# Performance work log

Measured on AMD Instinct MI355X. Metric: run time of the kernel, lower is better.

Reference implementation:

```python
import jax, jax.numpy as jnp
import numpy as np

N_HEAD = 16

def setup_inputs() -> dict:
    key = jax.random.key(0)
    k0, k1, k2, k3, k4 = jax.random.split(key, 5)
    B, T, C = 4, 2048, 1024
    x = jax.random.normal(k0, (B, T, C), dtype=jnp.float32)
    # torch nn.Linear weights are (out_features, in_features); scale like kaiming-uniform-ish
    s = 1.0 / np.sqrt(C)
    Wk = jax.random.uniform(k1, (C, C), jnp.float32, -s, s)
    Wq = jax.random.uniform(k2, (C, C), jnp.float32, -s, s)
    Wv = jax.random.uniform(k3, (C, C), jnp.float32, -s, s)
    Wo = jax.random.uniform(k4, (C, C), jnp.float32, -s, s)
    return {"x": x, "Wk": Wk, "Wq": Wq, "Wv": Wv, "Wo": Wo}

def reference(x, Wk, Wq, Wv, Wo):
    B, T, C = x.shape
    hs = C // N_HEAD
    # projections (torch Linear: y = x @ W.T), split heads -> (B, nh, T, hs)
    def proj(W):
        return (x @ W.T).reshape(B, T, N_HEAD, hs).transpose(0, 2, 1, 3)
    k = proj(Wk)
    q = proj(Wq)
    v = proj(Wv)
    # dot attention: scale by sqrt(head_dim) (k.shape[2] after transpose in source)
    score = jnp.einsum('bhqd,bhkd->bhqk', q, k) / jnp.sqrt(jnp.asarray(hs, x.dtype))
    # NOTE: source calls score.masked_fill(mask, -inf) without assignment -> mask has no effect.
    e = jax.nn.softmax(score, axis=-1)
    o = jnp.einsum('bhqk,bhkd->bhqd', e, v)          # (B, nh, T, hs)
    o = o.transpose(0, 2, 1, 3).reshape(B, T, C)     # merge heads
    o = o @ Wo.T                                      # final projection
    # dropout is identity in eval mode
    return o
```

## Files before the change

kernel.cpp:

```cpp
#include <hip/hip_runtime.h>
#include <hip/hip_bf16.h>
#include <cstddef>
#include <cstdint>

#define B_DIM 4
#define T_DIM 2048
#define C_DIM 1024
#define NHEAD 16
#define HS    64
#define QKV_LD 3072

#define QSCALE 0.18033688011112042f

typedef __attribute__((ext_vector_type(8))) short short8;
typedef __attribute__((ext_vector_type(4))) short short4v;
typedef __attribute__((ext_vector_type(4))) float f32x4;

__device__ __forceinline__ short f2bf(float x) {
    __hip_bfloat16 b = __float2bfloat16(x);
    return *reinterpret_cast<short*>(&b);
}

__device__ __forceinline__ void load_lds16(const void* g, void* l) {
    __builtin_amdgcn_global_load_lds(
        (const __attribute__((address_space(1))) void*)(g),
        (__attribute__((address_space(3))) void*)(l),
        16, 0, 0);
}

#define XBLK 4096
#define WBLK 512

__global__ __launch_bounds__(256) void cast_all(
    const float* __restrict__ x,
    const float* __restrict__ wq, const float* __restrict__ wk,
    const float* __restrict__ wv, const float* __restrict__ wo,
    short* __restrict__ xb, short* __restrict__ wout)
{
    const int bid = blockIdx.x;
    const float* in;
    short* out;
    float scale;
    int i;
    if (bid < XBLK) {
        i = bid * 256 + threadIdx.x;
        in = x; out = xb; scale = 1.0f;
    } else {
        const int r = bid - XBLK;
        const int sel = r >> 9;
        i = (r & (WBLK - 1)) * 256 + threadIdx.x;
        in  = (sel == 0) ? wq : (sel == 1) ? wk : (sel == 2) ? wv : wo;
        out = wout + (size_t)sel * (WBLK * 256 * 8);
        scale = (sel == 0) ? QSCALE : 1.0f;
    }
    const float4* p = (const float4*)in + (size_t)i * 2;
    float4 a = p[0], b = p[1];
    short8 o;
    o[0]=f2bf(a.x*scale); o[1]=f2bf(a.y*scale); o[2]=f2bf(a.z*scale); o[3]=f2bf(a.w*scale);
    o[4]=f2bf(b.x*scale); o[5]=f2bf(b.y*scale); o[6]=f2bf(b.z*scale); o[7]=f2bf(b.w*scale);
    *((short8*)out + i) = o;
}

template<int OUT_MODE>
__global__ __launch_bounds__(512, 2) void gemm_bt_8ph(
    const short* __restrict__ A,
    const short* __restrict__ Bm,
    void* __restrict__ Cm,
    short* __restrict__ Vt,
    int M, int N, int K)
{
    __shared__ __align__(16) short lds[49152];

    const int nbx = N >> 8;
    int wg = blockIdx.x;
    const int cpx = gridDim.x >> 3;
    wg = (wg & 7) * cpx + (wg >> 3);
    const int bx = wg % nbx, by = wg / nbx;
    const int m0 = by << 7, n0 = bx << 8;

    const int t = threadIdx.x;
    const int w = t >> 6, lane = t & 63;
    const int l16 = lane & 15, quad = lane >> 4;
    const int wm = w >> 2, wn = w & 3;

    const int rcall  = t >> 3;
    const int schunk = (t & 7) ^ (rcall & 7);
    const int dstoff = w * 512;

    const short* Ag = A  + (size_t)(m0 + rcall) * K + schunk * 8;
    const short* Bg = Bm + (size_t)(n0 + rcall) * K + schunk * 8;

    short* const Ab0 = lds;
    short* const Ab1 = lds + 8192;
    short* const Bb0 = lds + 16384;
    short* const Bb1 = lds + 32768;

    int aoff[4][2], boff[4][2];
    #pragma unroll
    for (int mf = 0; mf < 4; ++mf) {
        const int ar = wm * 64 + mf * 16 + l16;
        #pragma unroll
        for (int ks = 0; ks < 2; ++ks)
            aoff[mf][ks] = ar * 64 + (((ks * 4 + quad) ^ (ar & 7)) * 8);
    }
    #pragma unroll
    for (int nf = 0; nf < 4; ++nf) {
        const int br = wn * 64 + nf * 16 + l16;
        #pragma unroll
        for (int ks = 0; ks < 2; ++ks)
            boff[nf][ks] = br * 64 + (((ks * 4 + quad) ^ (br & 7)) * 8);
    }

    f32x4 acc[4][4];
    const f32x4 zero4 = {0.f, 0.f, 0.f, 0.f};
    #pragma unroll
    for (int mf = 0; mf < 4; ++mf)
        #pragma unroll
        for (int nf = 0; nf < 4; ++nf) acc[mf][nf] = zero4;

    const int NT = K >> 6;

    #define ST64(gb, kt, ro, lb)                                               \
        load_lds16((gb) + (size_t)(ro) * K + (size_t)(kt) * 64,                \
                   (lb) + (ro) * 64 + dstoff)

    ST64(Ag, 0, 0, Ab0); ST64(Ag, 0, 64, Ab0);
    ST64(Bg, 0, 0, Bb0); ST64(Bg, 0, 64, Bb0);
    ST64(Bg, 0, 128, Bb0); ST64(Bg, 0, 192, Bb0);
    ST64(Ag, 1, 0, Ab1); ST64(Ag, 1, 64, Ab1);

    for (int kt = 0; kt < NT; ++kt) {
        short* Acur = (kt & 1) ? Ab1 : Ab0;
        short* Bcur = (kt & 1) ? Bb1 : Bb0;
        short* Bnx  = (kt & 1) ? Bb0 : Bb1;

        if (kt == NT - 1) asm volatile("s_waitcnt vmcnt(0)" ::: "memory");
        else              asm volatile("s_waitcnt vmcnt(2)" ::: "memory");
        __builtin_amdgcn_s_barrier();

        short8 bfr[4][2], af[2][2];
        #pragma unroll
        for (int nf = 0; nf < 4; ++nf)
            #pragma unroll
            for (int ks = 0; ks < 2; ++ks)
                bfr[nf][ks] = *(const short8*)(Bcur + boff[nf][ks]);
        #pragma unroll
        for (int mf = 0; mf < 2; ++mf)
            #pragma unroll
            for (int ks = 0; ks < 2; ++ks)
                af[mf][ks] = *(const short8*)(Acur + aoff[mf][ks]);

        if (kt + 1 < NT) { ST64(Bg, kt + 1, 0, Bnx); ST64(Bg, kt + 1, 64, Bnx); }

        __builtin_amdgcn_s_barrier();
        __builtin_amdgcn_s_setprio(1);
        #pragma unroll
        for (int mf = 0; mf < 2; ++mf)
            #pragma unroll
            for (int nf = 0; nf < 4; ++nf)
                #pragma unroll
                for (int ks = 0; ks < 2; ++ks)
                    acc[mf][nf] = __builtin_amdgcn_mfma_f32_16x16x32_bf16(
                        af[mf][ks], bfr[nf][ks], acc[mf][nf], 0, 0, 0);
        __builtin_amdgcn_s_setprio(0);
        __builtin_amdgcn_s_barrier();

        short8 af2[2][2];
        #pragma unroll
        for (int mf = 0; mf < 2; ++mf)
            #pragma unroll
            for (int ks = 0; ks < 2; ++ks)
                af2[mf][ks] = *(const short8*)(Acur + aoff[2 + mf][ks]);

        if (kt + 1 < NT) { ST64(Bg, kt + 1, 128, Bnx); ST64(Bg, kt + 1, 192, Bnx); }

        __builtin_amdgcn_s_barrier();
        __builtin_amdgcn_s_setprio(1);
        #pragma unroll
        for (int mf = 0; mf < 2; ++mf)
            #pragma unroll
            for (int nf = 0; nf < 4; ++nf)
                #pragma unroll
                for (int ks = 0; ks < 2; ++ks)
                    acc[2 + mf][nf] = __builtin_amdgcn_mfma_f32_16x16x32_bf16(
                        af2[mf][ks], bfr[nf][ks], acc[2 + mf][nf], 0, 0, 0);
        __builtin_amdgcn_s_setprio(0);
        __builtin_amdgcn_s_barrier();

        if (kt + 2 < NT) {
            short* Aw = (kt & 1) ? Ab1 : Ab0;
            ST64(Ag, kt + 2, 0, Aw); ST64(Ag, kt + 2, 64, Aw);
        }
    }
    #undef ST64

    if (OUT_MODE == 2 && n0 >= 2 * C_DIM) {
        const int b    = m0 >> 11;
        const int tt0  = (m0 & 2047) + wm * 64 + quad * 4;
        #pragma unroll
        for (int nf = 0; nf < 4; ++nf) {
            const int vcol = (n0 - 2 * C_DIM) + wn * 64 + nf * 16 + l16;
            const int h    = vcol >> 6;
            const int d    = vcol & 63;
            short* dcol = Vt + ((size_t)((b << 4) + h) * HS + d) * T_DIM;
            #pragma unroll
            for (int mf = 0; mf < 4; ++mf) {
                const int tt = tt0 + mf * 16;
                short4v o;
                o[0] = f2bf(acc[mf][nf][0]); o[1] = f2bf(acc[mf][nf][1]);
                o[2] = f2bf(acc[mf][nf][2]); o[3] = f2bf(acc[mf][nf][3]);
                *(short4v*)(dcol + tt) = o;
            }
        }
    } else {
        #pragma unroll
        for (int mf = 0; mf < 4; ++mf) {
            const int row_base = m0 + wm * 64 + mf * 16 + quad * 4;
            #pragma unroll
            for (int nf = 0; nf < 4; ++nf) {
                const int col = n0 + wn * 64 + nf * 16 + l16;
                #pragma unroll
                for (int r = 0; r < 4; ++r) {
                    const size_t idx = (size_t)(row_base + r) * N + col;
                    if (OUT_MODE != 0) ((short*)Cm)[idx] = f2bf(acc[mf][nf][r]);
                    else               ((float*)Cm)[idx] = acc[mf][nf][r];
                }
            }
        }
    }
}

#define QSUB 2

__global__ __launch_bounds__(256, 4) void attn_mfma3(
    const short* __restrict__ Qb,
    const short* __restrict__ Kb,
    const short* __restrict__ Vt,
    short* __restrict__ O)
{
    const int bid  = blockIdx.x;
    const int slot = bid >> 3;
    const int head = ((bid & 7) << 3) + (slot >> 4);
    const int i0   = (slot & 15) * (64 * QSUB);
    const int b = head >> 4, h = head & 15;

    const int t    = threadIdx.x;
    const int w    = t >> 6;
    const int lane = t & 63;
    const int l16  = lane & 15;
    const int quad = lane >> 4;

    __shared__ short Ks[2][64][72];
    __shared__ short Vts[2][64][72];

    short8 qf[QSUB][2];
    #pragma unroll
    for (int sub = 0; sub < QSUB; ++sub) {
        const short* qrow = Qb
            + ((size_t)(b * T_DIM) + i0 + sub * 64 + w * 16 + l16) * QKV_LD + h * HS;
        qf[sub][0] = *(const short8*)(qrow + quad * 8);
        qf[sub][1] = *(const short8*)(qrow + 32 + quad * 8);
    }

    short8 onesv;
    #pragma unroll
    for (int j = 0; j < 8; ++j) onesv[j] = (short)0x3F80;

    const f32x4 zero4 = {0.f, 0.f, 0.f, 0.f};
    f32x4 oacc[QSUB][4];
    f32x4 lacc[QSUB];
    #pragma unroll
    for (int sub = 0; sub < QSUB; ++sub) {
        #pragma unroll
        for (int dg = 0; dg < 4; ++dg) oacc[sub][dg] = zero4;
        lacc[sub] = zero4;
    }

    const int sr = t >> 2;
    const int sc = (t & 3) * 16;
    const int krow = (sr & 32) | ((sr & 4) << 2) | ((sr & 24) >> 1) | (sr & 3);
    const short* kgbase = Kb + (size_t)(b * T_DIM) * QKV_LD + h * HS;
    const short* vgbase = Vt + ((size_t)head * HS + sr) * T_DIM;

    short8 kr0, kr1, vr0, vr1;
    {
        const short* kp = kgbase + (size_t)sr * QKV_LD + sc;
        kr0 = *(const short8*)kp;
        kr1 = *(const short8*)(kp + 8);
        vr0 = *(const short8*)(vgbase + sc);
        vr1 = *(const short8*)(vgbase + sc + 8);
    }

    const int NT = T_DIM / 64;
    for (int kt2 = 0; kt2 < NT; ++kt2) {
        const int buf = kt2 & 1;

        *(short8*)&Ks[buf][krow][sc]     = kr0;
        *(short8*)&Ks[buf][krow][sc + 8] = kr1;
        *(short8*)&Vts[buf][sr][sc]      = vr0;
        *(short8*)&Vts[buf][sr][sc + 8]  = vr1;
        __syncthreads();

        if (kt2 + 1 < NT) {
            const int j1 = (kt2 + 1) * 64;
            const short* kp = kgbase + (size_t)(j1 + sr) * QKV_LD + sc;
            kr0 = *(const short8*)kp;
            kr1 = *(const short8*)(kp + 8);
            const short* vp = vgbase + j1;
            vr0 = *(const short8*)(vp + sc);
            vr1 = *(const short8*)(vp + sc + 8);
        }

        short8 ka[4][2], va[4][2];
        #pragma unroll
        for (int kt = 0; kt < 4; ++kt) {
            ka[kt][0] = *(const short8*)&Ks[buf][kt * 16 + l16][quad * 8];
            ka[kt][1] = *(const short8*)&Ks[buf][kt * 16 + l16][32 + quad * 8];
            va[kt][0] = *(const short8*)&Vts[buf][kt * 16 + l16][quad * 8];
            va[kt][1] = *(const short8*)&Vts[buf][kt * 16 + l16][32 + quad * 8];
        }

        #pragma unroll
        for (int sub = 0; sub < QSUB; ++sub) {
            f32x4 s[4];
            #pragma unroll
            for (int kt = 0; kt < 4; ++kt) {
                f32x4 acc = zero4;
                acc = __builtin_amdgcn_mfma_f32_16x16x32_bf16(ka[kt][0], qf[sub][0], acc, 0, 0, 0);
                acc = __builtin_amdgcn_mfma_f32_16x16x32_bf16(ka[kt][1], qf[sub][1], acc, 0, 0, 0);
                s[kt] = acc;
            }

            short8 pa[2];
            #pragma unroll
            for (int hh = 0; hh < 2; ++hh) {
                #pragma unroll
                for (int c = 0; c < 2; ++c) {
                    f32x4 sv = s[2 * hh + c];
                    #pragma unroll
                    for (int r = 0; r < 4; ++r) {
                        float p = __builtin_amdgcn_exp2f(sv[r]);
                        pa[hh][c * 4 + r] = f2bf(p);
                    }
                }
            }

            lacc[sub] = __builtin_amdgcn_mfma_f32_16x16x32_bf16(pa[0], onesv, lacc[sub], 0, 0, 0);
            lacc[sub] = __builtin_amdgcn_mfma_f32_16x16x32_bf16(pa[1], onesv, lacc[sub], 0, 0, 0);

            #pragma unroll
            for (int dg = 0; dg < 4; ++dg) {
                oacc[sub][dg] = __builtin_amdgcn_mfma_f32_16x16x32_bf16(pa[0], va[dg][0], oacc[sub][dg], 0, 0, 0);
                oacc[sub][dg] = __builtin_amdgcn_mfma_f32_16x16x32_bf16(pa[1], va[dg][1], oacc[sub][dg], 0, 0, 0);
            }
        }
    }

    #pragma unroll
    for (int sub = 0; sub < QSUB; ++sub) {
        float linv[4];
        #pragma unroll
        for (int r = 0; r < 4; ++r) linv[r] = 1.0f / lacc[sub][r];

        #pragma unroll
        for (int r = 0; r < 4; ++r) {
            short* orow = O + ((size_t)(b * T_DIM) + i0 + sub * 64 + w * 16 + quad * 4 + r) * C_DIM + h * HS;
            #pragma unroll
            for (int dg = 0; dg < 4; ++dg)
                orow[dg * 16 + l16] = f2bf(oacc[sub][dg][r] * linv[r]);
        }
    }
}

extern "C" void kernel_launch(void* const* d_in, const int* in_sizes, int n_in,
                              void* d_out, int out_size, void* d_ws, size_t ws_size,
                              hipStream_t stream) {
    const float* x  = (const float*)d_in[0];
    const float* Wk = (const float*)d_in[1];
    const float* Wq = (const float*)d_in[2];
    const float* Wv = (const float*)d_in[3];
    const float* Wo = (const float*)d_in[4];
    float* out = (float*)d_out;

    const int M = B_DIM * T_DIM;
    const size_t NE = (size_t)M * C_DIM;
    const size_t NB = 2 * NE;
    const size_t WB = (size_t)2 * C_DIM * C_DIM;

    char* ws = (char*)d_ws;
    short* xb   = (short*)(ws);
    short* Ob   = xb;
    short* QKVb = (short*)(ws + NB);
    short* Vtb  = (short*)(ws + 4 * NB);
    short* W3b  = (short*)(ws + 5 * NB);
    short* Wob  = (short*)(ws + 5 * NB + 3 * WB);

    cast_all<<<dim3(XBLK + 4 * WBLK), 256, 0, stream>>>(
        x, Wq, Wk, Wv, Wo, xb, W3b);

    gemm_bt_8ph<2><<<dim3((QKV_LD / 256) * (M / 128)), 512, 0, stream>>>(
        xb, W3b, QKVb, Vtb, M, QKV_LD, C_DIM);

    attn_mfma3<<<dim3(T_DIM / (64 * QSUB) * B_DIM * NHEAD), 256, 0, stream>>>(
        QKVb, QKVb + C_DIM, Vtb, Ob);

    gemm_bt_8ph<0><<<dim3((C_DIM / 256) * (M / 128)), 512, 0, stream>>>(
        Ob, Wob, out, nullptr, M, C_DIM, C_DIM);
}
```

Baseline: 254.8 us.

## Restructure GEMM to 4 waves with 128x64 per-wave tiles and K=32 steps

Replaces the 512-thread, 8-wave GEMM (each wave owning 64x64 of a 128x256 tile, K step 64, split into two phases) with a 256-thread, 4-wave kernel in which each wave covers all 128 rows and 64 columns, using a K step of 32. A and B tiles for step kt+2 are prefetched into the buffer just consumed, with one barrier pair per step instead of four. The aim is fewer barriers and more MFMA work per LDS fragment load. In exchange it doubles the accumulator registers per thread, halves the waves per block, and doubles the number of K iterations.

```diff
diff --git a/kernel.cpp b/kernel.cpp
--- a/kernel.cpp
+++ b/kernel.cpp
@@ -62,14 +62,18 @@
 }
 
 template<int OUT_MODE>
-__global__ __launch_bounds__(512, 2) void gemm_bt_8ph(
+__global__ __launch_bounds__(256, 2) void gemm_bt_wide(
     const short* __restrict__ A,
     const short* __restrict__ Bm,
     void* __restrict__ Cm,
     short* __restrict__ Vt,
     int M, int N, int K)
 {
-    __shared__ __align__(16) short lds[49152];
+    __shared__ __align__(16) short lds[24576];
+    short* const Ab0 = lds;
+    short* const Ab1 = lds + 4096;
+    short* const Bb0 = lds + 8192;
+    short* const Bb1 = lds + 16384;
 
     const int nbx = N >> 8;
     int wg = blockIdx.x;
@@ -81,130 +85,89 @@
     const int t = threadIdx.x;
     const int w = t >> 6, lane = t & 63;
     const int l16 = lane & 15, quad = lane >> 4;
-    const int wm = w >> 2, wn = w & 3;
-
-    const int rcall  = t >> 3;
-    const int schunk = (t & 7) ^ (rcall & 7);
-    const int dstoff = w * 512;
-
+
+    const int rcall  = t >> 2;
+    const int schunk = (t & 3) ^ (rcall & 3);
     const short* Ag = A  + (size_t)(m0 + rcall) * K + schunk * 8;
     const short* Bg = Bm + (size_t)(n0 + rcall) * K + schunk * 8;
 
-    short* const Ab0 = lds;
-    short* const Ab1 = lds + 8192;
-    short* const Bb0 = lds + 16384;
-    short* const Bb1 = lds + 32768;
-
-    int aoff[4][2], boff[4][2];
-    #pragma unroll
-    for (int mf = 0; mf < 4; ++mf) {
-        const int ar = wm * 64 + mf * 16 + l16;
-        #pragma unroll
-        for (int ks = 0; ks < 2; ++ks)
-            aoff[mf][ks] = ar * 64 + (((ks * 4 + quad) ^ (ar & 7)) * 8);
+    int aoff[8], boff[4];
+    #pragma unroll
+    for (int mf = 0; mf < 8; ++mf) {
+        const int ar = mf * 16 + l16;
+        aoff[mf] = ar * 32 + ((quad ^ (ar & 3)) * 8);
     }
     #pragma unroll
     for (int nf = 0; nf < 4; ++nf) {
-        const int br = wn * 64 + nf * 16 + l16;
-        #pragma unroll
-        for (int ks = 0; ks < 2; ++ks)
-            boff[nf][ks] = br * 64 + (((ks * 4 + quad) ^ (br & 7)) * 8);
-    }
-
-    f32x4 acc[4][4];
+        const int br = w * 64 + nf * 16 + l16;
+        boff[nf] = br * 32 + ((quad ^ (br & 3)) * 8);
+    }
+
+    f32x4 acc[8][4];
     const f32x4 zero4 = {0.f, 0.f, 0.f, 0.f};
     #pragma unroll
-    for (int mf = 0; mf < 4; ++mf)
+    for (int mf = 0; mf < 8; ++mf)
         #pragma unroll
         for (int nf = 0; nf < 4; ++nf) acc[mf][nf] = zero4;
 
-    const int NT = K >> 6;
-
-    #define ST64(gb, kt, ro, lb)                                               \
-        load_lds16((gb) + (size_t)(ro) * K + (size_t)(kt) * 64,                \
-                   (lb) + (ro) * 64 + dstoff)
-
-    ST64(Ag, 0, 0, Ab0); ST64(Ag, 0, 64, Ab0);
-    ST64(Bg, 0, 0, Bb0); ST64(Bg, 0, 64, Bb0);
-    ST64(Bg, 0, 128, Bb0); ST64(Bg, 0, 192, Bb0);
-    ST64(Ag, 1, 0, Ab1); ST64(Ag, 1, 64, Ab1);
+    const int NT = K >> 5;
+
+    #define STW(gb, kt, ro, lb)                                                \
+        load_lds16((gb) + (size_t)(ro) * K + (size_t)(kt) * 32,                \
+                   (lb) + (ro) * 32 + w * 512)
+
+    STW(Ag, 0, 0, Ab0); STW(Ag, 0, 64, Ab0);
+    STW(Bg, 0, 0, Bb0); STW(Bg, 0, 64, Bb0);
+    STW(Bg, 0, 128, Bb0); STW(Bg, 0, 192, Bb0);
+    STW(Ag, 1, 0, Ab1); STW(Ag, 1, 64, Ab1);
+    STW(Bg, 1, 0, Bb1); STW(Bg, 1, 64, Bb1);
+    STW(Bg, 1, 128, Bb1); STW(Bg, 1, 192, Bb1);
 
     for (int kt = 0; kt < NT; ++kt) {
-        short* Acur = (kt & 1) ? Ab1 : Ab0;
-        short* Bcur = (kt & 1) ? Bb1 : Bb0;
-        short* Bnx  = (kt & 1) ? Bb0 : Bb1;
+        short* Ac = (kt & 1) ? Ab1 : Ab0;
+        short* Bc = (kt & 1) ? Bb1 : Bb0;
 
         if (kt == NT - 1) asm volatile("s_waitcnt vmcnt(0)" ::: "memory");
-        else              asm volatile("s_waitcnt vmcnt(2)" ::: "memory");
+        else              asm volatile("s_waitcnt vmcnt(6)" ::: "memory");
         __builtin_amdgcn_s_barrier();
 
-        short8 bfr[4][2], af[2][2];
-        #pragma unroll
-        for (int nf = 0; nf < 4; ++nf)
-            #pragma unroll
-            for (int ks = 0; ks < 2; ++ks)
-                bfr[nf][ks] = *(const short8*)(Bcur + boff[nf][ks]);
-        #pragma unroll
-        for (int mf = 0; mf < 2; ++mf)
-            #pragma unroll
-            for (int ks = 0; ks < 2; ++ks)
-                af[mf][ks] = *(const short8*)(Acur + aoff[mf][ks]);
-
-        if (kt + 1 < NT) { ST64(Bg, kt + 1, 0, Bnx); ST64(Bg, kt + 1, 64, Bnx); }
-
+        short8 af[8], bfr[4];
+        #pragma unroll
+        for (int mf = 0; mf < 8; ++mf) af[mf] = *(const short8*)(Ac + aoff[mf]);
+        #pragma unroll
+        for (int nf = 0; nf < 4; ++nf) bfr[nf] = *(const short8*)(Bc + boff[nf]);
+
+        asm volatile("s_waitcnt lgkmcnt(0)" ::: "memory");
         __builtin_amdgcn_s_barrier();
+
+        if (kt + 2 < NT) {
+            STW(Ag, kt + 2, 0, Ac); STW(Ag, kt + 2, 64, Ac);
+            STW(Bg, kt + 2, 0, Bc); STW(Bg, kt + 2, 64, Bc);
+            STW(Bg, kt + 2, 128, Bc); STW(Bg, kt + 2, 192, Bc);
+        }
+
         __builtin_amdgcn_s_setprio(1);
         #pragma unroll
-        for (int mf = 0; mf < 2; ++mf)
+        for (int mf = 0; mf < 8; ++mf)
             #pragma unroll
             for (int nf = 0; nf < 4; ++nf)
-                #pragma unroll
-                for (int ks = 0; ks < 2; ++ks)
-                    acc[mf][nf] = __builtin_amdgcn_mfma_f32_16x16x32_bf16(
-                        af[mf][ks], bfr[nf][ks], acc[mf][nf], 0, 0, 0);
+                acc[mf][nf] = __builtin_amdgcn_mfma_f32_16x16x32_bf16(
+                    af[mf], bfr[nf], acc[mf][nf], 0, 0, 0);
         __builtin_amdgcn_s_setprio(0);
-        __builtin_amdgcn_s_barrier();
-
-        short8 af2[2][2];
-        #pragma unroll
-        for (int mf = 0; mf < 2; ++mf)
-            #pragma unroll
-            for (int ks = 0; ks < 2; ++ks)
-                af2[mf][ks] = *(const short8*)(Acur + aoff[2 + mf][ks]);
-
-        if (kt + 1 < NT) { ST64(Bg, kt + 1, 128, Bnx); ST64(Bg, kt + 1, 192, Bnx); }
-
-        __builtin_amdgcn_s_barrier();
-        __builtin_amdgcn_s_setprio(1);
-        #pragma unroll
-        for (int mf = 0; mf < 2; ++mf)
-            #pragma unroll
-            for (int nf = 0; nf < 4; ++nf)
-                #pragma unroll
-                for (int ks = 0; ks < 2; ++ks)
-                    acc[2 + mf][nf] = __builtin_amdgcn_mfma_f32_16x16x32_bf16(
-                        af2[mf][ks], bfr[nf][ks], acc[2 + mf][nf], 0, 0, 0);
-        __builtin_amdgcn_s_setprio(0);
-        __builtin_amdgcn_s_barrier();
-
-        if (kt + 2 < NT) {
-            short* Aw = (kt & 1) ? Ab1 : Ab0;
-            ST64(Ag, kt + 2, 0, Aw); ST64(Ag, kt + 2, 64, Aw);
-        }
-    }
-    #undef ST64
+    }
+    #undef STW
 
     if (OUT_MODE == 2 && n0 >= 2 * C_DIM) {
-        const int b    = m0 >> 11;
-        const int tt0  = (m0 & 2047) + wm * 64 + quad * 4;
+        const int b   = m0 >> 11;
+        const int tt0 = (m0 & 2047) + quad * 4;
         #pragma unroll
         for (int nf = 0; nf < 4; ++nf) {
-            const int vcol = (n0 - 2 * C_DIM) + wn * 64 + nf * 16 + l16;
+            const int vcol = (n0 - 2 * C_DIM) + w * 64 + nf * 16 + l16;
             const int h    = vcol >> 6;
             const int d    = vcol & 63;
             short* dcol = Vt + ((size_t)((b << 4) + h) * HS + d) * T_DIM;
             #pragma unroll
-            for (int mf = 0; mf < 4; ++mf) {
+            for (int mf = 0; mf < 8; ++mf) {
                 const int tt = tt0 + mf * 16;
                 short4v o;
                 o[0] = f2bf(acc[mf][nf][0]); o[1] = f2bf(acc[mf][nf][1]);
@@ -214,11 +177,11 @@
         }
     } else {
         #pragma unroll
-        for (int mf = 0; mf < 4; ++mf) {
-            const int row_base = m0 + wm * 64 + mf * 16 + quad * 4;
+        for (int mf = 0; mf < 8; ++mf) {
+            const int row_base = m0 + mf * 16 + quad * 4;
             #pragma unroll
             for (int nf = 0; nf < 4; ++nf) {
-                const int col = n0 + wn * 64 + nf * 16 + l16;
+                const int col = n0 + w * 64 + nf * 16 + l16;
                 #pragma unroll
                 for (int r = 0; r < 4; ++r) {
                     const size_t idx = (size_t)(row_base + r) * N + col;
@@ -398,12 +361,12 @@
     cast_all<<<dim3(XBLK + 4 * WBLK), 256, 0, stream>>>(
         x, Wq, Wk, Wv, Wo, xb, W3b);
 
-    gemm_bt_8ph<2><<<dim3((QKV_LD / 256) * (M / 128)), 512, 0, stream>>>(
+    gemm_bt_wide<2><<<dim3((QKV_LD / 256) * (M / 128)), 256, 0, stream>>>(
         xb, W3b, QKVb, Vtb, M, QKV_LD, C_DIM);
 
     attn_mfma3<<<dim3(T_DIM / (64 * QSUB) * B_DIM * NHEAD), 256, 0, stream>>>(
         QKVb, QKVb + C_DIM, Vtb, Ob);
 
-    gemm_bt_8ph<0><<<dim3((C_DIM / 256) * (M / 128)), 512, 0, stream>>>(
+    gemm_bt_wide<0><<<dim3((C_DIM / 256) * (M / 128)), 256, 0, stream>>>(
         Ob, Wob, out, nullptr, M, C_DIM, C_DIM);
 }
```

After: 252.1 us. Within noise of the previous version (-1.0%).

## Add 4-wave wide-tile GEMM kernel for the QKV projection

Applied to the files above, without the earlier changes.

Adds a new GEMM kernel for the QKV projection that uses 256 threads (4 waves) per 128x256 tile. Each wave owns all 128 rows and 64 columns, so it holds 8x4 accumulators and reuses A fragments across more MFMAs. It uses a simpler double-buffered K=32 pipeline with smaller LDS. The old 8-wave kernel drops its V-transpose epilogue and is now used only for the output projection. The trade-off is higher register pressure and fewer waves for latency hiding, in exchange for fewer LDS reads per MFMA.

```diff
diff --git a/kernel.cpp b/kernel.cpp
--- a/kernel.cpp
+++ b/kernel.cpp
@@ -62,6 +62,138 @@
 }
 
 template<int OUT_MODE>
+__global__ __launch_bounds__(256, 2) void gemm_bt_wide(
+    const short* __restrict__ A,
+    const short* __restrict__ Bm,
+    void* __restrict__ Cm,
+    short* __restrict__ Vt,
+    int M, int N, int K)
+{
+    __shared__ __align__(16) short lds[24576];
+    short* const Ab0 = lds;
+    short* const Ab1 = lds + 4096;
+    short* const Bb0 = lds + 8192;
+    short* const Bb1 = lds + 16384;
+
+    const int nbx = N >> 8;
+    int wg = blockIdx.x;
+    const int cpx = gridDim.x >> 3;
+    wg = (wg & 7) * cpx + (wg >> 3);
+    const int bx = wg % nbx, by = wg / nbx;
+    const int m0 = by << 7, n0 = bx << 8;
+
+    const int t = threadIdx.x;
+    const int w = t >> 6, lane = t & 63;
+    const int l16 = lane & 15, quad = lane >> 4;
+
+    const int rcall  = t >> 2;
+    const int schunk = (t & 3) ^ (rcall & 3);
+    const short* Ag = A  + (size_t)(m0 + rcall) * K + schunk * 8;
+    const short* Bg = Bm + (size_t)(n0 + rcall) * K + schunk * 8;
+
+    int aoff[8], boff[4];
+    #pragma unroll
+    for (int mf = 0; mf < 8; ++mf) {
+        const int ar = mf * 16 + l16;
+        aoff[mf] = ar * 32 + ((quad ^ (ar & 3)) * 8);
+    }
+    #pragma unroll
+    for (int nf = 0; nf < 4; ++nf) {
+        const int br = w * 64 + nf * 16 + l16;
+        boff[nf] = br * 32 + ((quad ^ (br & 3)) * 8);
+    }
+
+    f32x4 acc[8][4];
+    const f32x4 zero4 = {0.f, 0.f, 0.f, 0.f};
+    #pragma unroll
+    for (int mf = 0; mf < 8; ++mf)
+        #pragma unroll
+        for (int nf = 0; nf < 4; ++nf) acc[mf][nf] = zero4;
+
+    const int NT = K >> 5;
+
+    #define STW(gb, kt, ro, lb)                                                \
+        load_lds16((gb) + (size_t)(ro) * K + (size_t)(kt) * 32,                \
+                   (lb) + (ro) * 32 + w * 512)
+
+    STW(Ag, 0, 0, Ab0); STW(Ag, 0, 64, Ab0);
+    STW(Bg, 0, 0, Bb0); STW(Bg, 0, 64, Bb0);
+    STW(Bg, 0, 128, Bb0); STW(Bg, 0, 192, Bb0);
+    STW(Ag, 1, 0, Ab1); STW(Ag, 1, 64, Ab1);
+    STW(Bg, 1, 0, Bb1); STW(Bg, 1, 64, Bb1);
+    STW(Bg, 1, 128, Bb1); STW(Bg, 1, 192, Bb1);
+
+    for (int kt = 0; kt < NT; ++kt) {
+        short* Ac = (kt & 1) ? Ab1 : Ab0;
+        short* Bc = (kt & 1) ? Bb1 : Bb0;
+
+        if (kt == NT - 1) asm volatile("s_waitcnt vmcnt(0)" ::: "memory");
+        else              asm volatile("s_waitcnt vmcnt(6)" ::: "memory");
+        __builtin_amdgcn_s_barrier();
+
+        short8 af[8], bfr[4];
+        #pragma unroll
+        for (int mf = 0; mf < 8; ++mf) af[mf] = *(const short8*)(Ac + aoff[mf]);
+        #pragma unroll
+        for (int nf = 0; nf < 4; ++nf) bfr[nf] = *(const short8*)(Bc + boff[nf]);
+
+        asm volatile("s_waitcnt lgkmcnt(0)" ::: "memory");
+        __builtin_amdgcn_s_barrier();
+
+        if (kt + 2 < NT) {
+            STW(Ag, kt + 2, 0, Ac); STW(Ag, kt + 2, 64, Ac);
+            STW(Bg, kt + 2, 0, Bc); STW(Bg, kt + 2, 64, Bc);
+            STW(Bg, kt + 2, 128, Bc); STW(Bg, kt + 2, 192, Bc);
+        }
+
+        __builtin_amdgcn_s_setprio(1);
+        #pragma unroll
+        for (int mf = 0; mf < 8; ++mf)
+            #pragma unroll
+            for (int nf = 0; nf < 4; ++nf)
+                acc[mf][nf] = __builtin_amdgcn_mfma_f32_16x16x32_bf16(
+                    af[mf], bfr[nf], acc[mf][nf], 0, 0, 0);
+        __builtin_amdgcn_s_setprio(0);
+    }
+    #undef STW
+
+    if (OUT_MODE == 2 && n0 >= 2 * C_DIM) {
+        const int b   = m0 >> 11;
+        const int tt0 = (m0 & 2047) + quad * 4;
+        #pragma unroll
+        for (int nf = 0; nf < 4; ++nf) {
+            const int vcol = (n0 - 2 * C_DIM) + w * 64 + nf * 16 + l16;
+            const int h    = vcol >> 6;
+            const int d    = vcol & 63;
+            short* dcol = Vt + ((size_t)((b << 4) + h) * HS + d) * T_DIM;
+            #pragma unroll
+            for (int mf = 0; mf < 8; ++mf) {
+                const int tt = tt0 + mf * 16;
+                short4v o;
+                o[0] = f2bf(acc[mf][nf][0]); o[1] = f2bf(acc[mf][nf][1]);
+                o[2] = f2bf(acc[mf][nf][2]); o[3] = f2bf(acc[mf][nf][3]);
+                *(short4v*)(dcol + tt) = o;
+            }
+        }
+    } else {
+        #pragma unroll
+        for (int mf = 0; mf < 8; ++mf) {
+            const int row_base = m0 + mf * 16 + quad * 4;
+            #pragma unroll
+            for (int nf = 0; nf < 4; ++nf) {
+                const int col = n0 + w * 64 + nf * 16 + l16;
+                #pragma unroll
+                for (int r = 0; r < 4; ++r) {
+                    const size_t idx = (size_t)(row_base + r) * N + col;
+                    if (OUT_MODE != 0) ((short*)Cm)[idx] = f2bf(acc[mf][nf][r]);
+                    else               ((float*)Cm)[idx] = acc[mf][nf][r];
+                }
+            }
+        }
+    }
+}
+
+template<int OUT_MODE>
 __global__ __launch_bounds__(512, 2) void gemm_bt_8ph(
     const short* __restrict__ A,
     const short* __restrict__ Bm,
@@ -194,37 +326,17 @@
     }
     #undef ST64
 
-    if (OUT_MODE == 2 && n0 >= 2 * C_DIM) {
-        const int b    = m0 >> 11;
-        const int tt0  = (m0 & 2047) + wm * 64 + quad * 4;
+    #pragma unroll
+    for (int mf = 0; mf < 4; ++mf) {
+        const int row_base = m0 + wm * 64 + mf * 16 + quad * 4;
         #pragma unroll
         for (int nf = 0; nf < 4; ++nf) {
-            const int vcol = (n0 - 2 * C_DIM) + wn * 64 + nf * 16 + l16;
-            const int h    = vcol >> 6;
-            const int d    = vcol & 63;
-            short* dcol = Vt + ((size_t)((b << 4) + h) * HS + d) * T_DIM;
-            #pragma unroll
-            for (int mf = 0; mf < 4; ++mf) {
-                const int tt = tt0 + mf * 16;
-                short4v o;
-                o[0] = f2bf(acc[mf][nf][0]); o[1] = f2bf(acc[mf][nf][1]);
-                o[2] = f2bf(acc[mf][nf][2]); o[3] = f2bf(acc[mf][nf][3]);
-                *(short4v*)(dcol + tt) = o;
-            }
-        }
-    } else {
-        #pragma unroll
-        for (int mf = 0; mf < 4; ++mf) {
-            const int row_base = m0 + wm * 64 + mf * 16 + quad * 4;
-            #pragma unroll
-            for (int nf = 0; nf < 4; ++nf) {
-                const int col = n0 + wn * 64 + nf * 16 + l16;
-                #pragma unroll
-                for (int r = 0; r < 4; ++r) {
-                    const size_t idx = (size_t)(row_base + r) * N + col;
-                    if (OUT_MODE != 0) ((short*)Cm)[idx] = f2bf(acc[mf][nf][r]);
-                    else               ((float*)Cm)[idx] = acc[mf][nf][r];
-                }
+            const int col = n0 + wn * 64 + nf * 16 + l16;
+            #pragma unroll
+            for (int r = 0; r < 4; ++r) {
+                const size_t idx = (size_t)(row_base + r) * N + col;
+                if (OUT_MODE != 0) ((short*)Cm)[idx] = f2bf(acc[mf][nf][r]);
+                else               ((float*)Cm)[idx] = acc[mf][nf][r];
             }
         }
     }
@@ -398,7 +510,7 @@
     cast_all<<<dim3(XBLK + 4 * WBLK), 256, 0, stream>>>(
         x, Wq, Wk, Wv, Wo, xb, W3b);
 
-    gemm_bt_8ph<2><<<dim3((QKV_LD / 256) * (M / 128)), 512, 0, stream>>>(
+    gemm_bt_wide<2><<<dim3((QKV_LD / 256) * (M / 128)), 256, 0, stream>>>(
         xb, W3b, QKVb, Vtb, M, QKV_LD, C_DIM);
 
     attn_mfma3<<<dim3(T_DIM / (64 * QSUB) * B_DIM * NHEAD), 256, 0, stream>>>(
```

Result: faster. 249.5 us (-2.1%).
